# Performance work log

Measured on AMD Instinct MI355X. Metric: run time of the kernel, lower is better.

The kernel has to match this reference:

```python
import jax, jax.numpy as jnp
import numpy as np

B, LQ, LK, D, H = 4, 1024, 1024, 512, 8


def setup_inputs() -> dict:
    key = jax.random.key(0)
    ks = jax.random.split(key, 6)
    # xavier_normal for (D, D): std = sqrt(2 / (D + D))
    std_qkv = (2.0 / (D + D)) ** 0.5
    std_p = (2.0 / (H * D + D)) ** 0.5
    x = jax.random.normal(ks[0], (B, LQ, D), dtype=jnp.float32)
    states = jax.random.normal(ks[1], (B, LK, D), dtype=jnp.float32)
    mask = jnp.ones((B, LQ, LK), dtype=jnp.int32)
    # per-head full-size QKV weights, stacked over heads: [H, D, D]
    Wq = jax.random.normal(ks[2], (H, D, D), dtype=jnp.float32) * std_qkv
    Wk = jax.random.normal(ks[3], (H, D, D), dtype=jnp.float32) * std_qkv
    Wv = jax.random.normal(ks[4], (H, D, D), dtype=jnp.float32) * std_qkv
    Wp = jax.random.normal(ks[5], (D, H * D), dtype=jnp.float32) * std_p
    return {"x": x, "states": states, "mask": mask,
            "Wq": Wq, "Wk": Wk, "Wv": Wv, "Wp": Wp}


def reference(x, states, mask, Wq, Wk, Wv, Wp):
    # Per-head linear projections (nn.Linear: y = x @ W.T), batched over heads.
    q = jnp.einsum('bld,hed->bhle', x, Wq)        # [B,H,Lq,D]
    k = jnp.einsum('bsd,hed->bhse', states, Wk)   # [B,H,Lk,D]
    v = jnp.einsum('bsd,hed->bhse', states, Wv)   # [B,H,Lk,D]
    scale = 1.0 / (D ** 0.5)
    scores = jnp.einsum('bhle,bhse->bhls', q, k) * scale  # [B,H,Lq,Lk]
    scores = jnp.where(mask[:, None, :, :] == 0, -jnp.inf, scores)
    attn = jax.nn.softmax(scores, axis=-1)
    # Original does broadcast multiply + sum; mathematically this is attn @ v.
    ctx = jnp.einsum('bhls,bhse->bhle', attn, v)  # [B,H,Lq,D]
    # torch.cat over heads in order -> head-major last dim
    ctx = jnp.transpose(ctx, (0, 2, 1, 3)).reshape(B, LQ, H * D)
    return ctx @ Wp.T  # [B,Lq,D]
```

## Files before the change

### kernel.cpp

```cpp
#include <hip/hip_runtime.h>
#include <hip/hip_bf16.h>
#include <cstdint>
#include <cstddef>


typedef __bf16 bf16;
typedef __bf16 bf16x4 __attribute__((ext_vector_type(4)));
typedef __bf16 bf16x8 __attribute__((ext_vector_type(8)));
typedef float f32x4 __attribute__((ext_vector_type(4)));

__device__ inline void gload_lds16(const void* g, void* l) {
  __builtin_amdgcn_global_load_lds(
      (const __attribute__((address_space(1))) void*)g,
      (__attribute__((address_space(3))) void*)l, 16, 0, 0);
}

template <typename CT, int MODE>
__device__ __forceinline__ void gemm_body(
    bf16* As, bf16* Bs,
    const bf16* __restrict__ A, const bf16* __restrict__ B, CT* __restrict__ C,
    int K, int lda, int ldb, int ldc, int m0, int n0, float scale,
    const unsigned* __restrict__ mrow, float* __restrict__ sumrow)
{
  const int t = threadIdx.x;
  const int lane = t & 63, w = t >> 6;
  const int wm = w >> 1, wn = w & 1;

  const int srow = t >> 3;
  const int schunk = (t & 7) ^ (srow & 7);
  const bf16* Ag = A + (size_t)(m0 + srow) * lda + schunk * 8;
  const bf16* Bg = B + (size_t)(n0 + srow) * ldb + schunk * 8;
  bf16* Als = As + t * 8;
  bf16* Bls = Bs + t * 8;

  f32x4 acc[4][4] = {};
  const int rr = lane & 15;
  const int q4 = lane >> 4;

  const int kIters = K >> 6;
  for (int kt = 0; kt < kIters; ++kt) {
    __syncthreads();
#pragma unroll
    for (int i = 0; i < 4; ++i) {
      gload_lds16(Ag + (size_t)(32 * i) * lda, Als + i * 2048);
      gload_lds16(Bg + (size_t)(32 * i) * ldb, Bls + i * 2048);
    }
    Ag += 64; Bg += 64;
    __syncthreads();

#pragma unroll
    for (int kk = 0; kk < 2; ++kk) {
      bf16x8 af[4], bfr[4];
      const int ck = kk * 4 + q4;
#pragma unroll
      for (int r = 0; r < 4; ++r) {
        const int R = wm * 64 + r * 16 + rr;
        af[r] = *(const bf16x8*)(As + R * 64 + ((ck ^ (R & 7)) << 3));
      }
#pragma unroll
      for (int c = 0; c < 4; ++c) {
        const int R = wn * 64 + c * 16 + rr;
        bfr[c] = *(const bf16x8*)(Bs + R * 64 + ((ck ^ (R & 7)) << 3));
      }
#pragma unroll
      for (int r = 0; r < 4; ++r)
#pragma unroll
        for (int c = 0; c < 4; ++c)
          acc[r][c] = __builtin_amdgcn_mfma_f32_16x16x32_bf16(af[r], bfr[c], acc[r][c], 0, 0, 0);
    }
  }

  if (MODE == 0) {
#pragma unroll
    for (int r = 0; r < 4; ++r) {
#pragma unroll
      for (int c = 0; c < 4; ++c) {
        const int gr0 = m0 + wm * 64 + r * 16 + (q4 << 2);
        const int gc = n0 + wn * 64 + c * 16 + rr;
#pragma unroll
        for (int i = 0; i < 4; ++i)
          C[(size_t)(gr0 + i) * ldc + gc] = (CT)(acc[r][c][i] * scale);
      }
    }
  } else {
    const int cb0 = (n0 + wn * 64) >> 5;
#pragma unroll
    for (int r = 0; r < 4; ++r) {
#pragma unroll
      for (int i = 0; i < 4; ++i) {
        const int row = m0 + wm * 64 + r * 16 + (q4 << 2) + i;
        const unsigned mw0 = mrow[(row << 5) + cb0];
        const unsigned mw1 = mrow[(row << 5) + cb0 + 1];
        float ps = 0.0f;
#pragma unroll
        for (int c = 0; c < 4; ++c) {
          const int gc = n0 + wn * 64 + c * 16 + rr;
          const unsigned mw = (c >= 2) ? mw1 : mw0;
          const unsigned bit = (mw >> (((c & 1) << 4) + rr)) & 1u;
          float p = bit ? __expf(acc[r][c][i] * scale) : 0.0f;
          C[(size_t)row * ldc + gc] = (CT)p;
          ps += p;
        }
        ps += __shfl_xor(ps, 1); ps += __shfl_xor(ps, 2);
        ps += __shfl_xor(ps, 4); ps += __shfl_xor(ps, 8);
        if (rr == 0) atomicAdd(sumrow + row, ps);
      }
    }
  }
}

__global__ __launch_bounds__(256) void prep_kernel(
    const float* __restrict__ x, const float* __restrict__ st,
    const float* __restrict__ Wq, const float* __restrict__ Wk,
    const float* __restrict__ Wp, const float* __restrict__ Wv,
    const int* __restrict__ mask,
    bf16* __restrict__ xb, bf16* __restrict__ stb, bf16* __restrict__ wqb,
    bf16* __restrict__ wkb, bf16* __restrict__ wpb, bf16* __restrict__ WvT,
    unsigned* __restrict__ mbits, float* __restrict__ sums)
{
  const int lin = blockIdx.x;
  const int t = threadIdx.x;
  if (lin < 10240) {
    const float* s; bf16* d;
    switch (lin >> 11) {
      case 0: s = x; d = xb; break;
      case 1: s = st; d = stb; break;
      case 2: s = Wq; d = wqb; break;
      case 3: s = Wk; d = wkb; break;
      default: s = Wp; d = wpb; break;
    }
    const int i = ((lin & 2047) * 256 + t) * 4;
    float4 v = *(const float4*)(s + i);
    bf16x4 o;
    o[0] = (bf16)v.x; o[1] = (bf16)v.y; o[2] = (bf16)v.z; o[3] = (bf16)v.w;
    *(bf16x4*)(d + i) = o;
  } else if (lin < 12288) {
    const int gid = (lin - 10240) * 256 + t;
    const int e0 = (gid & 127) * 4;
    const int d = (gid >> 7) & 511;
    const int h = gid >> 16;
    const float* src = Wv + (size_t)h * 262144 + (size_t)e0 * 512 + d;
    bf16x4 o;
    o[0] = (bf16)src[0];
    o[1] = (bf16)src[512];
    o[2] = (bf16)src[1024];
    o[3] = (bf16)src[1536];
    *(bf16x4*)(WvT + (size_t)h * 262144 + (size_t)d * 512 + e0) = o;
  } else if (lin < 12800) {
    const int gid = (lin - 12288) * 256 + t;
    const int* src = mask + (size_t)gid * 32;
    unsigned bits = 0;
#pragma unroll
    for (int j = 0; j < 32; j += 4) {
      int4 v = *(const int4*)(src + j);
      if (v.x) bits |= 1u << j;
      if (v.y) bits |= 1u << (j + 1);
      if (v.z) bits |= 1u << (j + 2);
      if (v.w) bits |= 1u << (j + 3);
    }
    mbits[gid] = bits;
  } else {
    const int i = ((lin - 12800) * 256 + t) * 4;
    *(float4*)(sums + i) = make_float4(0.f, 0.f, 0.f, 0.f);
  }
}

__global__ __launch_bounds__(256) void proj_kernel(
    const bf16* __restrict__ xb, const bf16* __restrict__ stb,
    const bf16* __restrict__ wqb, const bf16* __restrict__ wkb,
    const bf16* __restrict__ wpb, const bf16* __restrict__ WvT,
    bf16* __restrict__ q, bf16* __restrict__ k, bf16* __restrict__ U)
{
  __shared__ bf16 As[128 * 64];
  __shared__ bf16 Bs[128 * 64];
  const int lin = blockIdx.x;
  if (lin < 2048) {
    const int g = ((lin >> 8) << 3) | (lin & 7);
    const int tile = (lin >> 3) & 31;
    const int job = g >> 5;
    const int zz = g & 31;
    const size_t zb = zz >> 3, zh = zz & 7;
    const bf16* Ain = (job == 0) ? xb : stb;
    const bf16* W = (job == 0) ? wqb : wkb;
    bf16* Cout = (job == 0) ? q : k;
    gemm_body<bf16, 0>(As, Bs, Ain + zb * 524288, W + zh * 262144,
        Cout + zb * 4194304 + zh * 524288, 512, 512, 512, 512,
        (tile >> 2) * 128, (tile & 3) * 128, 1.0f, nullptr, nullptr);
  } else {
    const int lin2 = lin - 2048;
    const int h = lin2 >> 4;
    const int tile = lin2 & 15;
    gemm_body<bf16, 0>(As, Bs, wpb + (size_t)h * 512, WvT + (size_t)h * 262144,
        U + (size_t)h * 262144, 512, 4096, 512, 512,
        (tile >> 2) * 128, (tile & 3) * 128, 1.0f, nullptr, nullptr);
  }
}

__global__ __launch_bounds__(256) void big_kernel(
    const bf16* __restrict__ q, const bf16* __restrict__ k,
    const bf16* __restrict__ U, const bf16* __restrict__ stb,
    bf16* __restrict__ P, bf16* __restrict__ VWT,
    const unsigned* __restrict__ mbits, float* __restrict__ sums, float scale)
{
  __shared__ bf16 As[128 * 64];
  __shared__ bf16 Bs[128 * 64];
  const int lin = blockIdx.x;
  if (lin < 2048) {
    const int z = ((lin >> 9) << 3) | (lin & 7);
    const int j = (lin >> 3) & 63;
    const int zb = z >> 3, zh = z & 7;
    const bf16* A = q + (size_t)zb * 4194304 + (size_t)zh * 524288;
    const bf16* B = k + (size_t)zb * 4194304 + (size_t)zh * 524288;
    bf16* C = P + (size_t)zb * 8388608 + (size_t)zh * 1048576;
    const unsigned* mrow = mbits + ((size_t)zb << 15);
    float* sumrow = sums + ((size_t)z << 10);
    gemm_body<bf16, 1>(As, Bs, A, B, C, 512, 512, 512, 1024,
                       (j >> 3) * 128, (j & 7) * 128, scale, mrow, sumrow);
  } else {
    const int lin2 = lin - 2048;
    const int z = ((lin2 >> 8) << 3) | (lin2 & 7);
    const int j = (lin2 >> 3) & 31;
    const int zb = z >> 3, zh = z & 7;
    gemm_body<bf16, 0>(As, Bs, U + (size_t)zh * 262144, stb + (size_t)zb * 524288,
        VWT + (size_t)zb * 4194304 + (size_t)zh * 524288, 512, 512, 512, 1024,
        (j >> 3) * 128, (j & 7) * 128, 1.0f, nullptr, nullptr);
  }
}

__global__ __launch_bounds__(256) void pvw_kernel(
    const bf16* __restrict__ P, const bf16* __restrict__ VWT,
    const float* __restrict__ sums, float* __restrict__ part)
{
  __shared__ bf16 As[128 * 64];
  __shared__ bf16 Bs[128 * 64];
  const int lin = blockIdx.x;
  const int z = ((lin >> 8) << 3) | (lin & 7);
  const int j = (lin >> 3) & 31;
  const int zb = z >> 2, hp = z & 3;
  const int m0 = (j >> 2) * 128, n0 = (j & 3) * 128;
  const int t = threadIdx.x;
  const int lane = t & 63, w = t >> 6;
  const int wm = w >> 1, wn = w & 1;
  const int srow = t >> 3, schunk = (t & 7) ^ (srow & 7);
  const int rr = lane & 15, q4 = lane >> 4;
  bf16* Als = As + t * 8;
  bf16* Bls = Bs + t * 8;

  f32x4 accO[4][4] = {};

#pragma unroll
  for (int hh = 0; hh < 2; ++hh) {
    const int h = hp * 2 + hh;
    const bf16* Ag = P + (size_t)zb * 8388608 + (size_t)h * 1048576
                       + (size_t)(m0 + srow) * 1024 + schunk * 8;
    const bf16* Bg = VWT + (size_t)zb * 4194304 + (size_t)h * 524288
                        + (size_t)(n0 + srow) * 1024 + schunk * 8;
    f32x4 acc[4][4] = {};
    for (int kt = 0; kt < 16; ++kt) {
      __syncthreads();
#pragma unroll
      for (int i = 0; i < 4; ++i) {
        gload_lds16(Ag + (size_t)(32 * i) * 1024, Als + i * 2048);
        gload_lds16(Bg + (size_t)(32 * i) * 1024, Bls + i * 2048);
      }
      Ag += 64; Bg += 64;
      __syncthreads();
#pragma unroll
      for (int kk = 0; kk < 2; ++kk) {
        bf16x8 af[4], bfr[4];
        const int ck = kk * 4 + q4;
#pragma unroll
        for (int r = 0; r < 4; ++r) {
          const int R = wm * 64 + r * 16 + rr;
          af[r] = *(const bf16x8*)(As + R * 64 + ((ck ^ (R & 7)) << 3));
        }
#pragma unroll
        for (int c = 0; c < 4; ++c) {
          const int R = wn * 64 + c * 16 + rr;
          bfr[c] = *(const bf16x8*)(Bs + R * 64 + ((ck ^ (R & 7)) << 3));
        }
#pragma unroll
        for (int r = 0; r < 4; ++r)
#pragma unroll
          for (int c = 0; c < 4; ++c)
            acc[r][c] = __builtin_amdgcn_mfma_f32_16x16x32_bf16(af[r], bfr[c], acc[r][c], 0, 0, 0);
      }
    }
    const float* srs = sums + ((size_t)zb * 8 + h) * 1024;
#pragma unroll
    for (int r = 0; r < 4; ++r) {
#pragma unroll
      for (int i = 0; i < 4; ++i) {
        const float inv = 1.0f / srs[m0 + wm * 64 + r * 16 + (q4 << 2) + i];
#pragma unroll
        for (int c = 0; c < 4; ++c)
          accO[r][c][i] += acc[r][c][i] * inv;
      }
    }
  }

  float* Cp = part + (size_t)hp * 2097152 + (size_t)zb * 524288;
#pragma unroll
  for (int r = 0; r < 4; ++r) {
#pragma unroll
    for (int c = 0; c < 4; ++c) {
      const int gr0 = m0 + wm * 64 + r * 16 + (q4 << 2);
      const int gc = n0 + wn * 64 + c * 16 + rr;
#pragma unroll
      for (int i = 0; i < 4; ++i)
        Cp[(size_t)(gr0 + i) * 512 + gc] = accO[r][c][i];
    }
  }
}

__global__ __launch_bounds__(256) void reduce4(
    const float* __restrict__ part, float* __restrict__ out)
{
  const size_t i = ((size_t)blockIdx.x * 256 + threadIdx.x) * 4;
  float4 a = *(const float4*)(part + i);
  float4 b = *(const float4*)(part + 2097152 + i);
  float4 c = *(const float4*)(part + 4194304 + i);
  float4 d = *(const float4*)(part + 6291456 + i);
  float4 o;
  o.x = (a.x + b.x) + (c.x + d.x);
  o.y = (a.y + b.y) + (c.y + d.y);
  o.z = (a.z + b.z) + (c.z + d.z);
  o.w = (a.w + b.w) + (c.w + d.w);
  *(float4*)(out + i) = o;
}

extern "C" void kernel_launch(void* const* d_in, const int* in_sizes, int n_in,
                              void* d_out, int out_size, void* d_ws, size_t ws_size,
                              hipStream_t stream) {
  const float* x    = (const float*)d_in[0];
  const float* st   = (const float*)d_in[1];
  const int*   mask = (const int*)d_in[2];
  const float* Wq   = (const float*)d_in[3];
  const float* Wk   = (const float*)d_in[4];
  const float* Wv   = (const float*)d_in[5];
  const float* Wp   = (const float*)d_in[6];
  float* out = (float*)d_out;

  char* ws = (char*)d_ws;
  const size_t MB = 1048576;
  bf16* xb  = (bf16*)(ws);
  bf16* stb = (bf16*)(ws + 4 * MB);
  bf16* wqb = (bf16*)(ws + 8 * MB);
  bf16* wkb = (bf16*)(ws + 12 * MB);
  bf16* wpb = (bf16*)(ws + 16 * MB);
  bf16* WvT = (bf16*)(ws + 20 * MB);
  bf16* U   = (bf16*)(ws + 24 * MB);
  bf16* q   = (bf16*)(ws + 28 * MB);
  bf16* k   = (bf16*)(ws + 60 * MB);
  bf16* VWT = (bf16*)(ws + 92 * MB);
  bf16* sc  = (bf16*)(ws + 124 * MB);
  unsigned* mbits = (unsigned*)(ws + 188 * MB);
  float*    sums  = (float*)(ws + 189 * MB);
  float*    part  = (float*)(ws + 28 * MB);

  dim3 blk(256);
  const float scale = 0.04419417382415922f;

  prep_kernel<<<dim3(12832), blk, 0, stream>>>(x, st, Wq, Wk, Wp, Wv, mask,
      xb, stb, wqb, wkb, wpb, WvT, mbits, sums);

  proj_kernel<<<dim3(2176), blk, 0, stream>>>(xb, stb, wqb, wkb, wpb, WvT,
      q, k, U);

  big_kernel<<<dim3(3072), blk, 0, stream>>>(q, k, U, stb, sc, VWT,
      mbits, sums, scale);

  pvw_kernel<<<dim3(512), blk, 0, stream>>>(sc, VWT, sums, part);

  reduce4<<<dim3(2048), blk, 0, stream>>>(part, out);
}
```

Before: 275.8 us.

## Widen GEMM tiles to 128x256 and replace partial reduce with atomic adds

```diff
diff --git a/kernel.cpp b/kernel.cpp
--- a/kernel.cpp
+++ b/kernel.cpp
@@ -15,13 +15,14 @@
       (__attribute__((address_space(3))) void*)l, 16, 0, 0);
 }
 
-template <typename CT, int MODE>
+template <int NT, typename CT, int MODE>
 __device__ __forceinline__ void gemm_body(
     bf16* As, bf16* Bs,
     const bf16* __restrict__ A, const bf16* __restrict__ B, CT* __restrict__ C,
     int K, int lda, int ldb, int ldc, int m0, int n0, float scale,
     const unsigned* __restrict__ mrow, float* __restrict__ sumrow)
 {
+  constexpr int NW = NT / 32;
   const int t = threadIdx.x;
   const int lane = t & 63, w = t >> 6;
   const int wm = w >> 1, wn = w & 1;
@@ -33,7 +34,7 @@
   bf16* Als = As + t * 8;
   bf16* Bls = Bs + t * 8;
 
-  f32x4 acc[4][4] = {};
+  f32x4 acc[4][NW] = {};
   const int rr = lane & 15;
   const int q4 = lane >> 4;
 
@@ -41,16 +42,17 @@
   for (int kt = 0; kt < kIters; ++kt) {
     __syncthreads();
 #pragma unroll
-    for (int i = 0; i < 4; ++i) {
+    for (int i = 0; i < 4; ++i)
       gload_lds16(Ag + (size_t)(32 * i) * lda, Als + i * 2048);
+#pragma unroll
+    for (int i = 0; i < NT / 32; ++i)
       gload_lds16(Bg + (size_t)(32 * i) * ldb, Bls + i * 2048);
-    }
     Ag += 64; Bg += 64;
     __syncthreads();
 
 #pragma unroll
     for (int kk = 0; kk < 2; ++kk) {
-      bf16x8 af[4], bfr[4];
+      bf16x8 af[4], bfr[NW];
       const int ck = kk * 4 + q4;
 #pragma unroll
       for (int r = 0; r < 4; ++r) {
@@ -58,14 +60,14 @@
         af[r] = *(const bf16x8*)(As + R * 64 + ((ck ^ (R & 7)) << 3));
       }
 #pragma unroll
-      for (int c = 0; c < 4; ++c) {
-        const int R = wn * 64 + c * 16 + rr;
+      for (int c = 0; c < NW; ++c) {
+        const int R = wn * (NT / 2) + c * 16 + rr;
         bfr[c] = *(const bf16x8*)(Bs + R * 64 + ((ck ^ (R & 7)) << 3));
       }
 #pragma unroll
       for (int r = 0; r < 4; ++r)
 #pragma unroll
-        for (int c = 0; c < 4; ++c)
+        for (int c = 0; c < NW; ++c)
           acc[r][c] = __builtin_amdgcn_mfma_f32_16x16x32_bf16(af[r], bfr[c], acc[r][c], 0, 0, 0);
     }
   }
@@ -74,29 +76,30 @@
 #pragma unroll
     for (int r = 0; r < 4; ++r) {
 #pragma unroll
-      for (int c = 0; c < 4; ++c) {
+      for (int c = 0; c < NW; ++c) {
         const int gr0 = m0 + wm * 64 + r * 16 + (q4 << 2);
-        const int gc = n0 + wn * 64 + c * 16 + rr;
+        const int gc = n0 + wn * (NT / 2) + c * 16 + rr;
 #pragma unroll
         for (int i = 0; i < 4; ++i)
           C[(size_t)(gr0 + i) * ldc + gc] = (CT)(acc[r][c][i] * scale);
       }
     }
   } else {
-    const int cb0 = (n0 + wn * 64) >> 5;
+    const int cb0 = (n0 + wn * (NT / 2)) >> 5;
 #pragma unroll
     for (int r = 0; r < 4; ++r) {
 #pragma unroll
       for (int i = 0; i < 4; ++i) {
         const int row = m0 + wm * 64 + r * 16 + (q4 << 2) + i;
-        const unsigned mw0 = mrow[(row << 5) + cb0];
-        const unsigned mw1 = mrow[(row << 5) + cb0 + 1];
+        unsigned mw[NW / 2];
+#pragma unroll
+        for (int j = 0; j < NW / 2; ++j)
+          mw[j] = mrow[(row << 5) + cb0 + j];
         float ps = 0.0f;
 #pragma unroll
-        for (int c = 0; c < 4; ++c) {
-          const int gc = n0 + wn * 64 + c * 16 + rr;
-          const unsigned mw = (c >= 2) ? mw1 : mw0;
-          const unsigned bit = (mw >> (((c & 1) << 4) + rr)) & 1u;
+        for (int c = 0; c < NW; ++c) {
+          const int gc = n0 + wn * (NT / 2) + c * 16 + rr;
+          const unsigned bit = (mw[c >> 1] >> (((c & 1) << 4) + rr)) & 1u;
           float p = bit ? __expf(acc[r][c][i] * scale) : 0.0f;
           C[(size_t)row * ldc + gc] = (CT)p;
           ps += p;
@@ -172,27 +175,27 @@
     bf16* __restrict__ q, bf16* __restrict__ k, bf16* __restrict__ U)
 {
   __shared__ bf16 As[128 * 64];
-  __shared__ bf16 Bs[128 * 64];
+  __shared__ bf16 Bs[256 * 64];
   const int lin = blockIdx.x;
-  if (lin < 2048) {
-    const int g = ((lin >> 8) << 3) | (lin & 7);
-    const int tile = (lin >> 3) & 31;
-    const int job = g >> 5;
-    const int zz = g & 31;
+  if (lin < 1024) {
+    const int jz = ((lin >> 7) << 3) | (lin & 7);
+    const int j = (lin >> 3) & 15;
+    const int job = jz >> 5;
+    const int zz = jz & 31;
     const size_t zb = zz >> 3, zh = zz & 7;
     const bf16* Ain = (job == 0) ? xb : stb;
     const bf16* W = (job == 0) ? wqb : wkb;
     bf16* Cout = (job == 0) ? q : k;
-    gemm_body<bf16, 0>(As, Bs, Ain + zb * 524288, W + zh * 262144,
+    gemm_body<256, bf16, 0>(As, Bs, Ain + zb * 524288, W + zh * 262144,
         Cout + zb * 4194304 + zh * 524288, 512, 512, 512, 512,
-        (tile >> 2) * 128, (tile & 3) * 128, 1.0f, nullptr, nullptr);
+        (j >> 1) * 128, (j & 1) * 256, 1.0f, nullptr, nullptr);
   } else {
-    const int lin2 = lin - 2048;
-    const int h = lin2 >> 4;
-    const int tile = lin2 & 15;
-    gemm_body<bf16, 0>(As, Bs, wpb + (size_t)h * 512, WvT + (size_t)h * 262144,
+    const int lin2 = lin - 1024;
+    const int h = lin2 >> 3;
+    const int j = lin2 & 7;
+    gemm_body<256, bf16, 0>(As, Bs, wpb + (size_t)h * 512, WvT + (size_t)h * 262144,
         U + (size_t)h * 262144, 512, 4096, 512, 512,
-        (tile >> 2) * 128, (tile & 3) * 128, 1.0f, nullptr, nullptr);
+        (j >> 1) * 128, (j & 1) * 256, 1.0f, nullptr, nullptr);
   }
 }
 
@@ -203,33 +206,33 @@
     const unsigned* __restrict__ mbits, float* __restrict__ sums, float scale)
 {
   __shared__ bf16 As[128 * 64];
-  __shared__ bf16 Bs[128 * 64];
+  __shared__ bf16 Bs[256 * 64];
   const int lin = blockIdx.x;
-  if (lin < 2048) {
-    const int z = ((lin >> 9) << 3) | (lin & 7);
-    const int j = (lin >> 3) & 63;
+  if (lin < 1024) {
+    const int z = ((lin >> 8) << 3) | (lin & 7);
+    const int j = (lin >> 3) & 31;
     const int zb = z >> 3, zh = z & 7;
     const bf16* A = q + (size_t)zb * 4194304 + (size_t)zh * 524288;
     const bf16* B = k + (size_t)zb * 4194304 + (size_t)zh * 524288;
     bf16* C = P + (size_t)zb * 8388608 + (size_t)zh * 1048576;
     const unsigned* mrow = mbits + ((size_t)zb << 15);
     float* sumrow = sums + ((size_t)z << 10);
-    gemm_body<bf16, 1>(As, Bs, A, B, C, 512, 512, 512, 1024,
-                       (j >> 3) * 128, (j & 7) * 128, scale, mrow, sumrow);
+    gemm_body<256, bf16, 1>(As, Bs, A, B, C, 512, 512, 512, 1024,
+                            (j >> 2) * 128, (j & 3) * 256, scale, mrow, sumrow);
   } else {
-    const int lin2 = lin - 2048;
-    const int z = ((lin2 >> 8) << 3) | (lin2 & 7);
-    const int j = (lin2 >> 3) & 31;
+    const int lin2 = lin - 1024;
+    const int z = ((lin2 >> 7) << 3) | (lin2 & 7);
+    const int j = (lin2 >> 3) & 15;
     const int zb = z >> 3, zh = z & 7;
-    gemm_body<bf16, 0>(As, Bs, U + (size_t)zh * 262144, stb + (size_t)zb * 524288,
+    gemm_body<256, bf16, 0>(As, Bs, U + (size_t)zh * 262144, stb + (size_t)zb * 524288,
         VWT + (size_t)zb * 4194304 + (size_t)zh * 524288, 512, 512, 512, 1024,
-        (j >> 3) * 128, (j & 7) * 128, 1.0f, nullptr, nullptr);
+        (j >> 2) * 128, (j & 3) * 256, 1.0f, nullptr, nullptr);
   }
 }
 
 __global__ __launch_bounds__(256) void pvw_kernel(
     const bf16* __restrict__ P, const bf16* __restrict__ VWT,
-    const float* __restrict__ sums, float* __restrict__ part)
+    const float* __restrict__ sums, float* __restrict__ out)
 {
   __shared__ bf16 As[128 * 64];
   __shared__ bf16 Bs[128 * 64];
@@ -299,7 +302,7 @@
     }
   }
 
-  float* Cp = part + (size_t)hp * 2097152 + (size_t)zb * 524288;
+  float* Cp = out + (size_t)zb * 524288;
 #pragma unroll
   for (int r = 0; r < 4; ++r) {
 #pragma unroll
@@ -308,25 +311,9 @@
       const int gc = n0 + wn * 64 + c * 16 + rr;
 #pragma unroll
       for (int i = 0; i < 4; ++i)
-        Cp[(size_t)(gr0 + i) * 512 + gc] = accO[r][c][i];
-    }
-  }
-}
-
-__global__ __launch_bounds__(256) void reduce4(
-    const float* __restrict__ part, float* __restrict__ out)
-{
-  const size_t i = ((size_t)blockIdx.x * 256 + threadIdx.x) * 4;
-  float4 a = *(const float4*)(part + i);
-  float4 b = *(const float4*)(part + 2097152 + i);
-  float4 c = *(const float4*)(part + 4194304 + i);
-  float4 d = *(const float4*)(part + 6291456 + i);
-  float4 o;
-  o.x = (a.x + b.x) + (c.x + d.x);
-  o.y = (a.y + b.y) + (c.y + d.y);
-  o.z = (a.z + b.z) + (c.z + d.z);
-  o.w = (a.w + b.w) + (c.w + d.w);
-  *(float4*)(out + i) = o;
+        atomicAdd(Cp + (size_t)(gr0 + i) * 512 + gc, accO[r][c][i]);
+    }
+  }
 }
 
 extern "C" void kernel_launch(void* const* d_in, const int* in_sizes, int n_in,
@@ -356,21 +343,20 @@
   bf16* sc  = (bf16*)(ws + 124 * MB);
   unsigned* mbits = (unsigned*)(ws + 188 * MB);
   float*    sums  = (float*)(ws + 189 * MB);
-  float*    part  = (float*)(ws + 28 * MB);
 
   dim3 blk(256);
   const float scale = 0.04419417382415922f;
 
+  hipMemsetAsync(d_out, 0, (size_t)out_size * sizeof(float), stream);
+
   prep_kernel<<<dim3(12832), blk, 0, stream>>>(x, st, Wq, Wk, Wp, Wv, mask,
       xb, stb, wqb, wkb, wpb, WvT, mbits, sums);
 
-  proj_kernel<<<dim3(2176), blk, 0, stream>>>(xb, stb, wqb, wkb, wpb, WvT,
+  proj_kernel<<<dim3(1088), blk, 0, stream>>>(xb, stb, wqb, wkb, wpb, WvT,
       q, k, U);
 
-  big_kernel<<<dim3(3072), blk, 0, stream>>>(q, k, U, stb, sc, VWT,
+  big_kernel<<<dim3(1536), blk, 0, stream>>>(q, k, U, stb, sc, VWT,
       mbits, sums, scale);
 
-  pvw_kernel<<<dim3(512), blk, 0, stream>>>(sc, VWT, sums, part);
-
-  reduce4<<<dim3(2048), blk, 0, stream>>>(part, out);
-}
+  pvw_kernel<<<dim3(512), blk, 0, stream>>>(sc, VWT, sums, out);
+}
```

Measured after the change: 391.0 us. 41.8% more time.
